# Optimization experiments

Hardware: AMD Instinct MI355X
Metric: run time of the kernel (lower is better)

The kernel has to match this reference:

```python
import jax, jax.numpy as jnp
import numpy as np


def setup_inputs() -> dict:
    key = jax.random.key(0)
    k1, k2, k3 = jax.random.split(key, 3)
    G, E, C, H, I = 1, 8, 2048, 1024, 4096
    x = jax.random.normal(k1, (G, E, C, H), dtype=jnp.float32)
    # init per module.reset_parameters: normal std sqrt(0.1/hidden) and sqrt(0.1/intermediate)
    wi = jax.random.normal(k2, (E, H, I), dtype=jnp.float32) * np.sqrt(0.1 / H)
    wo = jax.random.normal(k3, (E, I, H), dtype=jnp.float32) * np.sqrt(0.1 / I)
    return {"x": x, "wi": wi, "wo": wo}


def reference(x, wi, wo):
    # x: [G, E, C, H] -> transpose to [E, G, C, H] -> [E, G*C, H]
    G, E, C, H = x.shape
    xt = jnp.swapaxes(x, 0, 1).reshape(E, G * C, H)
    # per-expert grouped GEMM: hidden -> intermediate, gelu, -> hidden
    h = jax.nn.gelu(jnp.einsum("eth,ehi->eti", xt, wi), approximate=False)
    out = jnp.einsum("eti,eih->eth", h, wo)
    out = out.reshape(E, G, C, H)
    return jnp.swapaxes(out, 0, 1)  # [G, E, C, H]
```

## Files before the change

### kernel.cpp

```cpp
#include <hip/hip_runtime.h>
#include <hip/hip_bf16.h>
#include <cstdint>

typedef __attribute__((ext_vector_type(4))) float f32x4;
typedef __attribute__((ext_vector_type(8))) short bf16x8;
typedef __attribute__((ext_vector_type(4))) short s16x4;
typedef __attribute__((ext_vector_type(8))) short s16x8;

__device__ __forceinline__ short f2bf(float f) {
    union { float f; unsigned u; } v; v.f = f;
    unsigned r = v.u + 0x7FFFu + ((v.u >> 16) & 1u);
    return (short)(r >> 16);
}

__global__ __launch_bounds__(256) void cast_bf16(const float* __restrict__ in,
                                                 short* __restrict__ out, long n) {
    long i = ((long)blockIdx.x * 256 + threadIdx.x) * 8;
    if (i + 7 < n) {
        float4 a = *(const float4*)(in + i);
        float4 b = *(const float4*)(in + i + 4);
        s16x8 o;
        o[0] = f2bf(a.x); o[1] = f2bf(a.y); o[2] = f2bf(a.z); o[3] = f2bf(a.w);
        o[4] = f2bf(b.x); o[5] = f2bf(b.y); o[6] = f2bf(b.z); o[7] = f2bf(b.w);
        *(s16x8*)(out + i) = o;
    }
}

__global__ __launch_bounds__(256) void transpose_cast(const float* __restrict__ in,
                                                      short* __restrict__ out,
                                                      int R, int C) {
    __shared__ float t[64][65];
    const size_t eoff = (size_t)blockIdx.z * R * C;
    in  += eoff;
    out += eoff;
    const int c0 = blockIdx.x * 64, r0 = blockIdx.y * 64;
    const int tid = threadIdx.x;
    const int rr  = tid >> 4;
    const int cc4 = (tid & 15) * 4;
    #pragma unroll
    for (int i = 0; i < 4; ++i) {
        const int row = i * 16 + rr;
        float4 v = *(const float4*)(in + (size_t)(r0 + row) * C + c0 + cc4);
        t[row][cc4 + 0] = v.x; t[row][cc4 + 1] = v.y;
        t[row][cc4 + 2] = v.z; t[row][cc4 + 3] = v.w;
    }
    __syncthreads();
    #pragma unroll
    for (int i = 0; i < 4; ++i) {
        const int oc = i * 16 + rr;
        s16x4 o;
        o[0] = f2bf(t[cc4 + 0][oc]);
        o[1] = f2bf(t[cc4 + 1][oc]);
        o[2] = f2bf(t[cc4 + 2][oc]);
        o[3] = f2bf(t[cc4 + 3][oc]);
        *(s16x4*)(out + (size_t)(c0 + oc) * R + r0 + cc4) = o;
    }
}

__device__ __forceinline__ void stage_tile64(const short* __restrict__ g,
                                             short* lds, int ld,
                                             int wave, int lane) {
    #pragma unroll
    for (int i = 0; i < 4; ++i) {
        const int c    = i * 256 + wave * 64 + lane;
        const int row  = c >> 3;
        const int slot = c & 7;
        const int gkc  = (slot ^ (row & 7)) << 3;
        const short* gp = g + (size_t)row * ld + gkc;
        short* lp = lds + (size_t)(i * 256 + wave * 64) * 8;
        __builtin_amdgcn_global_load_lds(
            (const __attribute__((address_space(1))) void*)gp,
            (__attribute__((address_space(3))) void*)lp, 16, 0, 0);
    }
}

template <int FUSE>
__global__ __launch_bounds__(256) void gemm_bt(const short* __restrict__ A,
                                               const short* __restrict__ Bt,
                                               void* __restrict__ Cout,
                                               int M, int N, int K) {
    __shared__ short As[128 * 64];
    __shared__ short Bs[128 * 64];
    const int tid  = threadIdx.x;
    const int lane = tid & 63;
    const int wave = tid >> 6;
    const int e    = blockIdx.z;
    A  += (size_t)e * M * K;
    Bt += (size_t)e * N * K;

    const int gridN = gridDim.x;
    const int lin   = blockIdx.y * gridN + blockIdx.x;
    const int band  = lin / (4 * gridN);
    const int rem   = lin - band * 4 * gridN;
    const int m0 = (band * 4 + (rem & 3)) * 128;
    const int n0 = (rem >> 2) * 128;

    const int wm = (wave >> 1) * 64;
    const int wn = (wave & 1) * 64;

    f32x4 acc[4][4] = {};

    const short* Ab = A  + (size_t)m0 * K;
    const short* Bb = Bt + (size_t)n0 * K;

    const int rA   = wm + (lane & 15);
    const int rB   = wn + (lane & 15);
    const int quad = lane >> 4;

    for (int k0 = 0; k0 < K; k0 += 64) {
        stage_tile64(Ab + k0, As, K, wave, lane);
        stage_tile64(Bb + k0, Bs, K, wave, lane);
        __syncthreads();

        #pragma unroll
        for (int s = 0; s < 2; ++s) {
            const int j = s * 4 + quad;
            bf16x8 af[4], bf[4];
            #pragma unroll
            for (int t = 0; t < 4; ++t) {
                const int ra = rA + t * 16;
                af[t] = *(const bf16x8*)&As[ra * 64 + ((j ^ (ra & 7)) << 3)];
            }
            #pragma unroll
            for (int t = 0; t < 4; ++t) {
                const int rb = rB + t * 16;
                bf[t] = *(const bf16x8*)&Bs[rb * 64 + ((j ^ (rb & 7)) << 3)];
            }
            #pragma unroll
            for (int i = 0; i < 4; ++i)
                #pragma unroll
                for (int jj = 0; jj < 4; ++jj)
                    acc[i][jj] = __builtin_amdgcn_mfma_f32_16x16x32_bf16(
                        af[i], bf[jj], acc[i][jj], 0, 0, 0);
        }
        __syncthreads();
    }

    const int r0 = quad << 2;
    const int cL = lane & 15;
    if (FUSE) {
        short* C = (short*)Cout + (size_t)e * M * N;
        #pragma unroll
        for (int i = 0; i < 4; ++i)
            #pragma unroll
            for (int j = 0; j < 4; ++j)
                #pragma unroll
                for (int r = 0; r < 4; ++r) {
                    const int row = m0 + wm + i * 16 + r0 + r;
                    const int col = n0 + wn + j * 16 + cL;
                    float v = acc[i][j][r];
                    v = 0.5f * v * (1.0f + erff(v * 0.70710678118654752f));
                    C[(size_t)row * N + col] = f2bf(v);
                }
    } else {
        float* C = (float*)Cout + (size_t)e * M * N;
        #pragma unroll
        for (int i = 0; i < 4; ++i)
            #pragma unroll
            for (int j = 0; j < 4; ++j)
                #pragma unroll
                for (int r = 0; r < 4; ++r) {
                    const int row = m0 + wm + i * 16 + r0 + r;
                    const int col = n0 + wn + j * 16 + cL;
                    C[(size_t)row * N + col] = acc[i][j][r];
                }
    }
}

extern "C" void kernel_launch(void* const* d_in, const int* in_sizes, int n_in,
                              void* d_out, int out_size, void* d_ws, size_t ws_size,
                              hipStream_t stream) {
    constexpr int E = 8, Ct = 2048, H = 1024, I = 4096;

    const float* x  = (const float*)d_in[0];
    const float* wi = (const float*)d_in[1];
    const float* wo = (const float*)d_in[2];
    float* out = (float*)d_out;

    char* ws = (char*)d_ws;
    short* xb  = (short*)(ws);
    short* wiT = (short*)(ws + (size_t)33554432);
    short* woT = (short*)(ws + (size_t)100663296);
    short* h   = (short*)(ws + (size_t)167772160);

    {
        long n = (long)E * Ct * H;
        cast_bf16<<<dim3((unsigned)(n / 2048)), dim3(256), 0, stream>>>(x, xb, n);
    }
    transpose_cast<<<dim3(I / 64, H / 64, E), dim3(256), 0, stream>>>(wi, wiT, H, I);
    transpose_cast<<<dim3(H / 64, I / 64, E), dim3(256), 0, stream>>>(wo, woT, I, H);

    gemm_bt<1><<<dim3(I / 128, Ct / 128, E), dim3(256), 0, stream>>>(
        xb, wiT, (void*)h, Ct, I, H);

    gemm_bt<0><<<dim3(H / 128, Ct / 128, E), dim3(256), 0, stream>>>(
        h, woT, (void*)out, Ct, H, I);
}
```

Measured before the change: 719.2 us.

## Merge prep kernels, stage GEMM epilogue through LDS, and interleave experts in FUSE grid

Measured after the change: 743.8 us. +3.4%, slower.

```diff
diff --git a/kernel.cpp b/kernel.cpp
--- a/kernel.cpp
+++ b/kernel.cpp
@@ -13,47 +13,59 @@
     return (short)(r >> 16);
 }
 
-__global__ __launch_bounds__(256) void cast_bf16(const float* __restrict__ in,
-                                                 short* __restrict__ out, long n) {
-    long i = ((long)blockIdx.x * 256 + threadIdx.x) * 8;
-    if (i + 7 < n) {
-        float4 a = *(const float4*)(in + i);
-        float4 b = *(const float4*)(in + i + 4);
+__device__ __forceinline__ float gelu_exact(float v) {
+    return 0.5f * v * (1.0f + erff(v * 0.70710678118654752f));
+}
+
+__global__ __launch_bounds__(256) void prep(const float* __restrict__ x,
+                                            const float* __restrict__ wi,
+                                            const float* __restrict__ wo,
+                                            short* __restrict__ xb,
+                                            short* __restrict__ wiT,
+                                            short* __restrict__ woT) {
+    __shared__ float t[64][65];
+    const int b = blockIdx.x, tid = threadIdx.x;
+    if (b < 8192) {
+        const long i = ((long)b * 256 + tid) * 8;
+        float4 a = *(const float4*)(x + i);
+        float4 c = *(const float4*)(x + i + 4);
         s16x8 o;
         o[0] = f2bf(a.x); o[1] = f2bf(a.y); o[2] = f2bf(a.z); o[3] = f2bf(a.w);
-        o[4] = f2bf(b.x); o[5] = f2bf(b.y); o[6] = f2bf(b.z); o[7] = f2bf(b.w);
-        *(s16x8*)(out + i) = o;
-    }
-}
-
-__global__ __launch_bounds__(256) void transpose_cast(const float* __restrict__ in,
-                                                      short* __restrict__ out,
-                                                      int R, int C) {
-    __shared__ float t[64][65];
-    const size_t eoff = (size_t)blockIdx.z * R * C;
-    in  += eoff;
-    out += eoff;
-    const int c0 = blockIdx.x * 64, r0 = blockIdx.y * 64;
-    const int tid = threadIdx.x;
-    const int rr  = tid >> 4;
-    const int cc4 = (tid & 15) * 4;
+        o[4] = f2bf(c.x); o[5] = f2bf(c.y); o[6] = f2bf(c.z); o[7] = f2bf(c.w);
+        *(s16x8*)(xb + i) = o;
+        return;
+    }
+    const float* in; short* out; int R, C, c0, r0;
+    if (b < 16384) {
+        const int b2 = b - 8192, e = b2 >> 10, tt = b2 & 1023;
+        R = 1024; C = 4096;
+        c0 = (tt & 63) * 64; r0 = (tt >> 6) * 64;
+        in  = wi  + (size_t)e * R * C;
+        out = wiT + (size_t)e * R * C;
+    } else {
+        const int b3 = b - 16384, e = b3 >> 10, tt = b3 & 1023;
+        R = 4096; C = 1024;
+        c0 = (tt & 15) * 64; r0 = (tt >> 4) * 64;
+        in  = wo  + (size_t)e * R * C;
+        out = woT + (size_t)e * R * C;
+    }
+    const int lr = tid >> 4, lc4 = (tid & 15) * 4;
     #pragma unroll
     for (int i = 0; i < 4; ++i) {
-        const int row = i * 16 + rr;
-        float4 v = *(const float4*)(in + (size_t)(r0 + row) * C + c0 + cc4);
-        t[row][cc4 + 0] = v.x; t[row][cc4 + 1] = v.y;
-        t[row][cc4 + 2] = v.z; t[row][cc4 + 3] = v.w;
+        const int row = i * 16 + lr;
+        float4 v = *(const float4*)(in + (size_t)(r0 + row) * C + c0 + lc4);
+        t[row][lc4 + 0] = v.x; t[row][lc4 + 1] = v.y;
+        t[row][lc4 + 2] = v.z; t[row][lc4 + 3] = v.w;
     }
     __syncthreads();
-    #pragma unroll
-    for (int i = 0; i < 4; ++i) {
-        const int oc = i * 16 + rr;
-        s16x4 o;
-        o[0] = f2bf(t[cc4 + 0][oc]);
-        o[1] = f2bf(t[cc4 + 1][oc]);
-        o[2] = f2bf(t[cc4 + 2][oc]);
-        o[3] = f2bf(t[cc4 + 3][oc]);
-        *(s16x4*)(out + (size_t)(c0 + oc) * R + r0 + cc4) = o;
+    const int rseg = (tid & 7) * 8;
+    #pragma unroll
+    for (int i = 0; i < 2; ++i) {
+        const int oc = i * 32 + (tid >> 3);
+        s16x8 o;
+        #pragma unroll
+        for (int j = 0; j < 8; ++j) o[j] = f2bf(t[rseg + j][oc]);
+        *(s16x8*)(out + (size_t)(c0 + oc) * R + r0 + rseg) = o;
     }
 }
 
@@ -79,21 +91,30 @@
                                                const short* __restrict__ Bt,
                                                void* __restrict__ Cout,
                                                int M, int N, int K) {
-    __shared__ short As[128 * 64];
-    __shared__ short Bs[128 * 64];
+    __shared__ __align__(16) short smem[2 * 128 * 64];
+    short* As = smem;
+    short* Bs = smem + 128 * 64;
     const int tid  = threadIdx.x;
     const int lane = tid & 63;
     const int wave = tid >> 6;
-    const int e    = blockIdx.z;
+
+    int e, m0, n0;
+    if (FUSE) {
+        e = blockIdx.x & 7;
+        const int r = blockIdx.x >> 3;
+        m0 = (r & 15) << 7;
+        n0 = (((r >> 6) << 2) + ((r >> 4) & 3)) << 7;
+    } else {
+        e = blockIdx.z;
+        const int gridN = gridDim.x;
+        const int lin   = blockIdx.y * gridN + blockIdx.x;
+        const int band  = lin / (4 * gridN);
+        const int rem   = lin - band * 4 * gridN;
+        m0 = (band * 4 + (rem & 3)) * 128;
+        n0 = (rem >> 2) * 128;
+    }
     A  += (size_t)e * M * K;
     Bt += (size_t)e * N * K;
-
-    const int gridN = gridDim.x;
-    const int lin   = blockIdx.y * gridN + blockIdx.x;
-    const int band  = lin / (4 * gridN);
-    const int rem   = lin - band * 4 * gridN;
-    const int m0 = (band * 4 + (rem & 3)) * 128;
-    const int n0 = (rem >> 2) * 128;
 
     const int wm = (wave >> 1) * 64;
     const int wn = (wave & 1) * 64;
@@ -136,34 +157,41 @@
         __syncthreads();
     }
 
-    const int r0 = quad << 2;
+    float* Lf = (float*)smem;
     const int cL = lane & 15;
-    if (FUSE) {
-        short* C = (short*)Cout + (size_t)e * M * N;
+    #pragma unroll
+    for (int p = 0; p < 4; ++p) {
+        if (p) __syncthreads();
         #pragma unroll
         for (int i = 0; i < 4; ++i)
             #pragma unroll
-            for (int j = 0; j < 4; ++j)
-                #pragma unroll
-                for (int r = 0; r < 4; ++r) {
-                    const int row = m0 + wm + i * 16 + r0 + r;
-                    const int col = n0 + wn + j * 16 + cL;
-                    float v = acc[i][j][r];
-                    v = 0.5f * v * (1.0f + erff(v * 0.70710678118654752f));
-                    C[(size_t)row * N + col] = f2bf(v);
-                }
-    } else {
-        float* C = (float*)Cout + (size_t)e * M * N;
-        #pragma unroll
-        for (int i = 0; i < 4; ++i)
-            #pragma unroll
-            for (int j = 0; j < 4; ++j)
-                #pragma unroll
-                for (int r = 0; r < 4; ++r) {
-                    const int row = m0 + wm + i * 16 + r0 + r;
-                    const int col = n0 + wn + j * 16 + cL;
-                    C[(size_t)row * N + col] = acc[i][j][r];
-                }
+            for (int r = 0; r < 4; ++r)
+                Lf[(wm + i * 16 + (quad << 2) + r) * 36 + (wave & 1) * 16 + cL]
+                    = acc[i][p][r];
+        __syncthreads();
+        #pragma unroll
+        for (int c2 = 0; c2 < 2; ++c2) {
+            const int id  = c2 * 256 + tid;
+            const int row = id >> 2;
+            const int cl  = (id & 3) * 8;
+            f32x4 v0 = *(const f32x4*)&Lf[row * 36 + cl];
+            f32x4 v1 = *(const f32x4*)&Lf[row * 36 + cl + 4];
+            const int grow = m0 + row;
+            const int gcol = n0 + ((cl & 16) ? 64 : 0) + p * 16 + (cl & 8);
+            if (FUSE) {
+                s16x8 o;
+                o[0] = f2bf(gelu_exact(v0[0])); o[1] = f2bf(gelu_exact(v0[1]));
+                o[2] = f2bf(gelu_exact(v0[2])); o[3] = f2bf(gelu_exact(v0[3]));
+                o[4] = f2bf(gelu_exact(v1[0])); o[5] = f2bf(gelu_exact(v1[1]));
+                o[6] = f2bf(gelu_exact(v1[2])); o[7] = f2bf(gelu_exact(v1[3]));
+                short* C = (short*)Cout + (size_t)e * M * N;
+                *(s16x8*)&C[(size_t)grow * N + gcol] = o;
+            } else {
+                float* C = (float*)Cout + (size_t)e * M * N;
+                *(f32x4*)&C[(size_t)grow * N + gcol]     = v0;
+                *(f32x4*)&C[(size_t)grow * N + gcol + 4] = v1;
+            }
+        }
     }
 }
 
@@ -183,14 +211,9 @@
     short* woT = (short*)(ws + (size_t)100663296);
     short* h   = (short*)(ws + (size_t)167772160);
 
-    {
-        long n = (long)E * Ct * H;
-        cast_bf16<<<dim3((unsigned)(n / 2048)), dim3(256), 0, stream>>>(x, xb, n);
-    }
-    transpose_cast<<<dim3(I / 64, H / 64, E), dim3(256), 0, stream>>>(wi, wiT, H, I);
-    transpose_cast<<<dim3(H / 64, I / 64, E), dim3(256), 0, stream>>>(wo, woT, I, H);
-
-    gemm_bt<1><<<dim3(I / 128, Ct / 128, E), dim3(256), 0, stream>>>(
+    prep<<<dim3(24576), dim3(256), 0, stream>>>(x, wi, wo, xb, wiT, woT);
+
+    gemm_bt<1><<<dim3(4096), dim3(256), 0, stream>>>(
         xb, wiT, (void*)h, Ct, I, H);
 
     gemm_bt<0><<<dim3(H / 128, Ct / 128, E), dim3(256), 0, stream>>>(
```
